# Kernel tuning notes

Hardware: AMD Instinct MI355X
Metric: run time of the kernel (lower is better)

Reference implementation:

```python
import jax, jax.numpy as jnp
import numpy as np

B, L, D_MODEL, D_STATE, D_CONV, EXPAND = 2, 1024, 1024, 16, 4, 2
D_INNER = D_MODEL * EXPAND


def setup_inputs() -> dict:
    key = jax.random.key(0)
    ks = jax.random.split(key, 8)
    s = lambda fan: 1.0 / np.sqrt(fan)
    x = jax.random.normal(ks[0], (B, L, D_MODEL), jnp.float32)
    in_proj_w = jax.random.normal(ks[1], (D_MODEL, 2 * D_INNER), jnp.float32) * s(D_MODEL)
    conv_w = jax.random.normal(ks[2], (D_INNER, 1, D_CONV), jnp.float32) * s(D_CONV)
    conv_b = jax.random.normal(ks[3], (D_INNER,), jnp.float32) * 0.01
    x_proj_w = jax.random.normal(ks[4], (D_INNER, 2 * D_STATE + D_INNER), jnp.float32) * s(D_INNER)
    dt_proj_w = jax.random.normal(ks[5], (D_INNER, D_INNER), jnp.float32) * s(D_INNER)
    dt_proj_b = jax.random.normal(ks[6], (D_INNER,), jnp.float32) * 0.01
    A_log = jnp.log(jnp.tile(jnp.arange(1, D_STATE + 1, dtype=jnp.float32)[None, :], (D_INNER, 1)))
    D = jnp.ones((D_INNER,), jnp.float32)
    out_proj_w = jax.random.normal(ks[7], (D_INNER, D_MODEL), jnp.float32) * s(D_INNER)
    return {"x": x, "in_proj_w": in_proj_w, "conv_w": conv_w, "conv_b": conv_b,
            "x_proj_w": x_proj_w, "dt_proj_w": dt_proj_w, "dt_proj_b": dt_proj_b,
            "A_log": A_log, "D": D, "out_proj_w": out_proj_w}


def _mamba_forward(x, in_proj_w, conv_w, conv_b, x_proj_w, dt_proj_w, dt_proj_b, A_log, D, out_proj_w):
    Bb, Ll, _ = x.shape
    d_inner, _, d_conv = conv_w.shape
    d_state = A_log.shape[1]
    # input projection and gate split
    xz = x @ in_proj_w                       # [B, L, 2*Di]
    x_inner, z = jnp.split(xz, 2, axis=-1)   # each [B, L, Di]
    # causal depthwise conv (left pad k-1, truncate to L == torch pad+slice)
    xc = jnp.transpose(x_inner, (0, 2, 1))   # [B, Di, L]
    xc = jax.lax.conv_general_dilated(
        xc, conv_w, window_strides=(1,), padding=[(d_conv - 1, 0)],
        dimension_numbers=("NCH", "OIH", "NCH"), feature_group_count=d_inner)
    xc = xc + conv_b[None, :, None]
    u = jax.nn.silu(jnp.transpose(xc, (0, 2, 1)))  # [B, L, Di]
    # SSM parameter projections
    ssm = u @ x_proj_w                        # [B, L, 2N+Di]
    B_ssm = ssm[..., :d_state]                # [B, L, N]
    C_ssm = ssm[..., d_state:2 * d_state]     # [B, L, N]
    dt = jax.nn.softplus(ssm[..., 2 * d_state:] @ dt_proj_w + dt_proj_b)  # [B, L, Di]
    A_real = -jnp.exp(A_log)                  # [Di, N]
    # selective scan over sequence (recurrence via lax.scan)
    def step(h, inp):
        dt_t, B_t, u_t = inp                  # [B,Di], [B,N], [B,Di]
        dA = jnp.exp(dt_t[..., None] * A_real)            # [B, Di, N]
        dBu = dt_t[..., None] * B_t[:, None, :] * u_t[..., None]
        h = dA * h + dBu
        return h, h
    h0 = jnp.zeros((Bb, d_inner, d_state), x.dtype)
    xs = (jnp.swapaxes(dt, 0, 1), jnp.swapaxes(B_ssm, 0, 1), jnp.swapaxes(u, 0, 1))
    _, states = jax.lax.scan(step, h0, xs)    # [L, B, Di, N]
    y = jnp.einsum("lbdn,lbn->lbd", states, jnp.swapaxes(C_ssm, 0, 1))
    y = jnp.swapaxes(y, 0, 1) + D * u         # skip connection
    y = y * jax.nn.silu(z)                    # gating
    return y @ out_proj_w                     # [B, L, d_model]


def reference(x, in_proj_w, conv_w, conv_b, x_proj_w, dt_proj_w, dt_proj_b, A_log, D, out_proj_w):
    return _mamba_forward(x, in_proj_w, conv_w, conv_b, x_proj_w, dt_proj_w, dt_proj_b, A_log, D, out_proj_w)
```

## Files before the change

kernel.cpp:

```cpp
#include <hip/hip_runtime.h>
#include <hip/hip_bf16.h>

#define BB 2
#define LL 1024
#define DMODEL 1024
#define DINNER 2048
#define DSTATE 16
#define DCONV 4
#define MM (BB * LL)
#define N_XZ 4096
#define N_SSM 2080
#define N_SSM_PAD 2176
#define CCH 32
#define LCH 32

typedef __hip_bfloat16 bf16;
typedef short bf16x8 __attribute__((ext_vector_type(8)));
typedef float f32x4 __attribute__((ext_vector_type(4)));

__device__ __forceinline__ void load16_lds(const bf16* g, bf16* l) {
    __builtin_amdgcn_global_load_lds(
        (const __attribute__((address_space(1))) void*)g,
        (__attribute__((address_space(3))) void*)l,
        16, 0, 0);
}

__global__ __launch_bounds__(256) void prep_kernel(
    const float* __restrict__ x, bf16* __restrict__ xbf,
    const float* __restrict__ w1, bf16* __restrict__ o1,
    const float* __restrict__ w2, bf16* __restrict__ o2,
    const float* __restrict__ w3, bf16* __restrict__ o3,
    const float* __restrict__ w4, bf16* __restrict__ o4)
{
    int bid = blockIdx.x;
    const float* src; bf16* dst; int K, N, tn, tk;
    if (bid < 4096)        { src = w1; dst = o1; K = 1024; N = 4096; tn = bid & 127; tk = bid >> 7; }
    else if (bid < 8256)   { bid -= 4096;  src = w2; dst = o2; K = 2048; N = 2080; tn = bid % 65; tk = bid / 65; }
    else if (bid < 12352)  { bid -= 8256;  src = w3; dst = o3; K = 2048; N = 2048; tn = bid & 63; tk = bid >> 6; }
    else if (bid < 14400)  { bid -= 12352; src = w4; dst = o4; K = 2048; N = 1024; tn = bid & 31; tk = bid >> 5; }
    else {
        bid -= 14400;
        int i = (bid * 256 + threadIdx.x) * 4;
        float4 v = *(const float4*)(x + i);
        xbf[i + 0] = __float2bfloat16(v.x);
        xbf[i + 1] = __float2bfloat16(v.y);
        xbf[i + 2] = __float2bfloat16(v.z);
        xbf[i + 3] = __float2bfloat16(v.w);
        return;
    }
    __shared__ float tile[32][33];
    const int nb = tn * 32, kb = tk * 32;
    const int tx = threadIdx.x & 31, ty = threadIdx.x >> 5;
    #pragma unroll
    for (int i = 0; i < 32; i += 8) {
        int k = kb + ty + i, n = nb + tx;
        tile[ty + i][tx] = (k < K && n < N) ? src[(size_t)k * N + n] : 0.f;
    }
    __syncthreads();
    #pragma unroll
    for (int i = 0; i < 32; i += 8) {
        int n = nb + ty + i, k = kb + tx;
        if (n < N && k < K) dst[(size_t)n * K + k] = __float2bfloat16(tile[tx][ty + i]);
    }
}

#define TM 128
#define TN 64
#define TK 64
template<int EPI, int KSPLIT = 1, int SWZ = -1>
__global__ __launch_bounds__(256) void mfma_gemm(
    const bf16* __restrict__ A, int lda,
    const bf16* __restrict__ Wt, int ldw,
    float* __restrict__ Cf, bf16* __restrict__ Cb, int ldc,
    const float* __restrict__ bias,
    int N, int K)
{
    __shared__ __align__(16) bf16 As[2][TM * TK];
    __shared__ __align__(16) bf16 Bs[2][TN * TK];
    const int tid = threadIdx.x;
    const int wave = tid >> 6, lane = tid & 63;
    const int wm = (wave >> 1) * 64, wn = (wave & 1) * 32;

    int bx, by;
    if (SWZ >= 0) {
        int id = blockIdx.x + (int)(gridDim.x * blockIdx.y);
        int xcd = id & 7, slot = id >> 3;
        bx = (xcd << SWZ) + (slot & ((1 << SWZ) - 1));
        by = slot >> SWZ;
    } else { bx = blockIdx.x; by = blockIdx.y; }
    const int m0 = by * TM, n0 = bx * TN;
    const int lm = lane & 15, kq = lane >> 4;

    const int srow = lane >> 3;
    const int schunk = (lane & 7) ^ srow;
    const bf16* gA = A + (size_t)(m0 + wave * 32 + srow) * lda + schunk * 8;
    const bf16* gB = Wt + (size_t)(n0 + wave * 16 + srow) * ldw + schunk * 8;

    const int Kc = K / KSPLIT;
    const int kbeg = (KSPLIT > 1) ? blockIdx.z * Kc : 0;
    const int NK = Kc / TK;

    f32x4 acc[4][2] = {};
    const int fsw = (lm & 7);

    auto stage = [&](int buf, int it) {
        const int k0 = kbeg + it * TK;
        bf16* lA = &As[buf][(wave * 32) * TK];
        bf16* lB = &Bs[buf][(wave * 16) * TK];
        #pragma unroll
        for (int g = 0; g < 4; ++g)
            load16_lds(gA + (size_t)(8 * g) * lda + k0, lA + (8 * g) * TK);
        #pragma unroll
        for (int g = 0; g < 2; ++g)
            load16_lds(gB + (size_t)(8 * g) * ldw + k0, lB + (8 * g) * TK);
    };
    auto compute = [&](int buf) {
        bf16x8 af[4][2], bfr[2][2];
        #pragma unroll
        for (int i = 0; i < 4; ++i)
            #pragma unroll
            for (int t = 0; t < 2; ++t)
                af[i][t] = *(const bf16x8*)(&As[buf][(wm + i * 16 + lm) * TK + ((t * 4 + kq) ^ fsw) * 8]);
        #pragma unroll
        for (int j = 0; j < 2; ++j)
            #pragma unroll
            for (int t = 0; t < 2; ++t)
                bfr[j][t] = *(const bf16x8*)(&Bs[buf][(wn + j * 16 + lm) * TK + ((t * 4 + kq) ^ fsw) * 8]);
        #pragma unroll
        for (int t = 0; t < 2; ++t)
            #pragma unroll
            for (int i = 0; i < 4; ++i)
                #pragma unroll
                for (int j = 0; j < 2; ++j)
                    acc[i][j] = __builtin_amdgcn_mfma_f32_16x16x32_bf16(af[i][t], bfr[j][t], acc[i][j], 0, 0, 0);
    };

    stage(0, 0);
    for (int it = 0; it < NK; it += 2) {
        stage(1, it + 1);
        __builtin_amdgcn_s_waitcnt(0x0F76);
        __builtin_amdgcn_s_barrier();
        compute(0);
        __builtin_amdgcn_s_barrier();
        if (it + 2 < NK) {
            stage(0, it + 2);
            __builtin_amdgcn_s_waitcnt(0x0F76);
        } else {
            __builtin_amdgcn_s_waitcnt(0x0F70);
        }
        __builtin_amdgcn_s_barrier();
        compute(1);
        __builtin_amdgcn_s_barrier();
    }

    #pragma unroll
    for (int i = 0; i < 4; ++i) {
        #pragma unroll
        for (int j = 0; j < 2; ++j) {
            int gcol = n0 + wn + j * 16 + lm;
            if ((EPI == 0 || EPI == 3) && gcol >= N) continue;
            #pragma unroll
            for (int r = 0; r < 4; ++r) {
                int grow = m0 + wm + i * 16 + kq * 4 + r;
                float v = acc[i][j][r];
                if (EPI == 1) {
                    v += bias[gcol];
                    v = (v > 20.f) ? v : log1pf(__expf(v));
                    Cf[(size_t)grow * ldc + gcol] = v;
                } else if (EPI == 2) {
                    if (KSPLIT > 1) atomicAdd(&Cf[(size_t)grow * ldc + gcol], v);
                    else            Cf[(size_t)grow * ldc + gcol] = v;
                } else if (EPI == 3) {
                    if (gcol < 32) Cf[(size_t)grow * 32 + gcol] = v;
                    else           Cb[(size_t)grow * ldc + gcol] = __float2bfloat16(v);
                } else {
                    Cb[(size_t)grow * ldc + gcol] = __float2bfloat16(v);
                }
            }
        }
    }
}

__global__ void conv_silu_kernel(const bf16* __restrict__ xz,
                                 const float* __restrict__ conv_w,
                                 const float* __restrict__ conv_b,
                                 bf16* __restrict__ u)
{
    int idx = blockIdx.x * blockDim.x + threadIdx.x;
    if (idx >= BB * LL * DINNER) return;
    int d = idx & (DINNER - 1);
    int l = (idx >> 11) & (LL - 1);
    int b = idx >> 21;
    float acc = conv_b[d];
    #pragma unroll
    for (int j = 0; j < DCONV; ++j) {
        int ll = l - (DCONV - 1) + j;
        if (ll >= 0) {
            float xv = (float)xz[((size_t)(b * LL + ll)) * N_XZ + d];
            acc = fmaf(conv_w[d * DCONV + j], xv, acc);
        }
    }
    u[idx] = __float2bfloat16(acc / (1.f + __expf(-acc)));
}

__global__ __launch_bounds__(256) void scan_phase_a(
    const float* __restrict__ dt, const bf16* __restrict__ u,
    const float* __restrict__ BC,
    const float* __restrict__ A_log,
    float* __restrict__ chunkP, float* __restrict__ chunkH)
{
    const int d = blockIdx.x * 256 + threadIdx.x;
    const int c = blockIdx.y, b = blockIdx.z;
    const int l0 = c * LCH;

    float A[DSTATE];
    {
        const f32x4* ap = (const f32x4*)(A_log + d * DSTATE);
        #pragma unroll
        for (int q = 0; q < 4; ++q) {
            f32x4 v = ap[q];
            #pragma unroll
            for (int r = 0; r < 4; ++r) A[q * 4 + r] = -__expf(v[r]);
        }
    }
    float h[DSTATE];
    #pragma unroll
    for (int n = 0; n < DSTATE; ++n) h[n] = 0.f;
    float sdt = 0.f;

    const float* dtp = dt + ((size_t)b * LL + l0) * DINNER + d;
    const bf16* up = u + ((size_t)b * LL + l0) * DINNER + d;
    const float* bcp = BC + ((size_t)b * LL + l0) * 32;

    #pragma unroll 2
    for (int i = 0; i < LCH; ++i) {
        float dtv = *dtp;
        float uv  = (float)*up;
        float du  = dtv * uv;
        f32x4 Bv[4];
        #pragma unroll
        for (int q = 0; q < 4; ++q) Bv[q] = *(const f32x4*)(bcp + q * 4);
        #pragma unroll
        for (int n = 0; n < DSTATE; ++n) {
            float a = __expf(dtv * A[n]);
            h[n] = fmaf(a, h[n], du * Bv[n >> 2][n & 3]);
        }
        sdt += dtv;
        dtp += DINNER; up += DINNER; bcp += 32;
    }

    size_t idx = (((size_t)b * CCH + c) * DINNER + d) * DSTATE;
    #pragma unroll
    for (int q = 0; q < 4; ++q) {
        f32x4 pv, hv;
        #pragma unroll
        for (int r = 0; r < 4; ++r) { pv[r] = __expf(A[q * 4 + r] * sdt); hv[r] = h[q * 4 + r]; }
        *(f32x4*)(chunkP + idx + q * 4) = pv;
        *(f32x4*)(chunkH + idx + q * 4) = hv;
    }
}

__global__ __launch_bounds__(256) void scan_phase_p(
    const float* __restrict__ chunkP, float* __restrict__ chunkH)
{
    int gid = blockIdx.x * 256 + threadIdx.x;
    int n = gid & 15;
    int d = (gid >> 4) & (DINNER - 1);
    int b = gid >> 15;
    const size_t stride = (size_t)DINNER * DSTATE;
    size_t idx = ((size_t)b * CCH * DINNER + d) * DSTATE + n;
    float H = 0.f;
    for (int c = 0; c < CCH; ++c) {
        float P  = chunkP[idx];
        float hl = chunkH[idx];
        chunkH[idx] = H;
        H = fmaf(P, H, hl);
        idx += stride;
    }
}

__global__ __launch_bounds__(256) void scan_phase_b(
    const float* __restrict__ dt, bf16* __restrict__ u,
    const float* __restrict__ BC, const bf16* __restrict__ xz,
    const float* __restrict__ A_log, const float* __restrict__ Dp,
    const float* __restrict__ chunkH)
{
    const int d = blockIdx.x * 256 + threadIdx.x;
    const int c = blockIdx.y, b = blockIdx.z;
    const int l0 = c * LCH;

    float A[DSTATE];
    {
        const f32x4* ap = (const f32x4*)(A_log + d * DSTATE);
        #pragma unroll
        for (int q = 0; q < 4; ++q) {
            f32x4 v = ap[q];
            #pragma unroll
            for (int r = 0; r < 4; ++r) A[q * 4 + r] = -__expf(v[r]);
        }
    }
    const float Dd = Dp[d];
    float h[DSTATE];
    {
        size_t idx = (((size_t)b * CCH + c) * DINNER + d) * DSTATE;
        #pragma unroll
        for (int q = 0; q < 4; ++q) {
            f32x4 v = *(const f32x4*)(chunkH + idx + q * 4);
            #pragma unroll
            for (int r = 0; r < 4; ++r) h[q * 4 + r] = v[r];
        }
    }

    const float* dtp = dt + ((size_t)b * LL + l0) * DINNER + d;
    bf16* up = u + ((size_t)b * LL + l0) * DINNER + d;
    const float* bcp = BC + ((size_t)b * LL + l0) * 32;
    const bf16* zp = xz + ((size_t)b * LL + l0) * N_XZ + DINNER + d;

    #pragma unroll 2
    for (int i = 0; i < LCH; ++i) {
        float dtv = *dtp;
        float uv  = (float)*up;
        float du  = dtv * uv;
        f32x4 Bv[4], Cv[4];
        #pragma unroll
        for (int q = 0; q < 4; ++q) {
            Bv[q] = *(const f32x4*)(bcp + q * 4);
            Cv[q] = *(const f32x4*)(bcp + 16 + q * 4);
        }
        float acc = 0.f;
        #pragma unroll
        for (int n = 0; n < DSTATE; ++n) {
            float a = __expf(dtv * A[n]);
            h[n] = fmaf(a, h[n], du * Bv[n >> 2][n & 3]);
            acc = fmaf(h[n], Cv[n >> 2][n & 3], acc);
        }
        float zv = (float)*zp;
        acc = fmaf(Dd, uv, acc);
        acc *= zv / (1.f + __expf(-zv));
        *up = __float2bfloat16(acc);
        dtp += DINNER; up += DINNER; bcp += 32; zp += N_XZ;
    }
}

extern "C" void kernel_launch(void* const* d_in, const int* in_sizes, int n_in,
                              void* d_out, int out_size, void* d_ws, size_t ws_size,
                              hipStream_t stream) {
    const float* x         = (const float*)d_in[0];
    const float* in_proj_w = (const float*)d_in[1];
    const float* conv_w    = (const float*)d_in[2];
    const float* conv_b    = (const float*)d_in[3];
    const float* x_proj_w  = (const float*)d_in[4];
    const float* dt_proj_w = (const float*)d_in[5];
    const float* dt_proj_b = (const float*)d_in[6];
    const float* A_log     = (const float*)d_in[7];
    const float* Dp        = (const float*)d_in[8];
    const float* out_proj_w= (const float*)d_in[9];
    float* out = (float*)d_out;

    char* p = (char*)d_ws;
    float* dt   = (float*)p;                          p += (size_t)MM * DINNER * 4;
    bf16*  xbf  = (bf16*)dt;
    bf16*  xz   = (bf16*)p;                           p += (size_t)MM * N_XZ * 2;
    bf16*  u    = (bf16*)p;                           p += (size_t)MM * DINNER * 2;
    bf16*  ssm  = (bf16*)p;                           p += (size_t)MM * N_SSM * 2;
    bf16*  Wt1  = (bf16*)p;                           p += (size_t)N_XZ * DMODEL * 2;
    bf16*  Wt2  = (bf16*)p;                           p += (size_t)N_SSM_PAD * DINNER * 2;
    bf16*  Wt3  = (bf16*)p;                           p += (size_t)DINNER * DINNER * 2;
    bf16*  Wt4  = (bf16*)p;                           p += (size_t)DMODEL * DINNER * 2;
    float* BC   = (float*)p;                          p += (size_t)MM * 32 * 4;
    float* chunkP = (float*)Wt1;
    float* chunkH = (float*)Wt2;

    prep_kernel<<<16448, 256, 0, stream>>>(x, xbf, in_proj_w, Wt1, x_proj_w, Wt2,
                                           dt_proj_w, Wt3, out_proj_w, Wt4);
    mfma_gemm<0, 1, 3><<<dim3(N_XZ / TN, MM / TM), 256, 0, stream>>>(
        xbf, DMODEL, Wt1, DMODEL, nullptr, xz, N_XZ, nullptr, N_XZ, DMODEL);
    {
        int n = BB * LL * DINNER;
        conv_silu_kernel<<<(n + 255) / 256, 256, 0, stream>>>(xz, conv_w, conv_b, u);
    }
    mfma_gemm<3><<<dim3(N_SSM_PAD / TN, MM / TM), 256, 0, stream>>>(
        u, DINNER, Wt2, DINNER, BC, ssm, N_SSM, nullptr, N_SSM, DINNER);
    mfma_gemm<1, 1, 2><<<dim3(DINNER / TN, MM / TM), 256, 0, stream>>>(
        ssm + 2 * DSTATE, N_SSM, Wt3, DINNER, dt, nullptr, DINNER, dt_proj_b, DINNER, DINNER);
    scan_phase_a<<<dim3(DINNER / 256, CCH, BB), 256, 0, stream>>>(dt, u, BC, A_log, chunkP, chunkH);
    scan_phase_p<<<dim3(BB * DINNER * DSTATE / 256), 256, 0, stream>>>(chunkP, chunkH);
    scan_phase_b<<<dim3(DINNER / 256, CCH, BB), 256, 0, stream>>>(dt, u, BC, xz, A_log, Dp, chunkH);
    hipMemsetAsync(out, 0, (size_t)out_size * sizeof(float), stream);
    mfma_gemm<2, 2, 1><<<dim3(DMODEL / TN, MM / TM, 2), 256, 0, stream>>>(
        u, DINNER, Wt4, DINNER, out, nullptr, DMODEL, nullptr, DMODEL, DINNER);
}
```

Baseline: 332.9 us.

## Use 2-wave GEMM blocks with 64x64 warp tiles and vectorize conv

The GEMM now runs two waves per block instead of four. Each wave computes a 64x64 sub-tile, so each wave issues more MFMAs per LDS fragment load and gets more register-level reuse. Each wave now stages twice as many global-to-LDS loads, and the waitcnt thresholds change to match. The depthwise conv+SiLU kernel is also vectorized to process 8 channels per thread with 16-byte loads and stores. The trade-off is higher register pressure and fewer waves per block for latency hiding.

```diff
diff --git a/kernel.cpp b/kernel.cpp
--- a/kernel.cpp
+++ b/kernel.cpp
@@ -68,7 +68,7 @@
 #define TN 64
 #define TK 64
 template<int EPI, int KSPLIT = 1, int SWZ = -1>
-__global__ __launch_bounds__(256) void mfma_gemm(
+__global__ __launch_bounds__(128) void mfma_gemm(
     const bf16* __restrict__ A, int lda,
     const bf16* __restrict__ Wt, int ldw,
     float* __restrict__ Cf, bf16* __restrict__ Cb, int ldc,
@@ -79,7 +79,7 @@
     __shared__ __align__(16) bf16 Bs[2][TN * TK];
     const int tid = threadIdx.x;
     const int wave = tid >> 6, lane = tid & 63;
-    const int wm = (wave >> 1) * 64, wn = (wave & 1) * 32;
+    const int wm = wave * 64;
 
     int bx, by;
     if (SWZ >= 0) {
@@ -93,58 +93,58 @@
 
     const int srow = lane >> 3;
     const int schunk = (lane & 7) ^ srow;
-    const bf16* gA = A + (size_t)(m0 + wave * 32 + srow) * lda + schunk * 8;
-    const bf16* gB = Wt + (size_t)(n0 + wave * 16 + srow) * ldw + schunk * 8;
+    const bf16* gA = A + (size_t)(m0 + wave * 64 + srow) * lda + schunk * 8;
+    const bf16* gB = Wt + (size_t)(n0 + wave * 32 + srow) * ldw + schunk * 8;
 
     const int Kc = K / KSPLIT;
     const int kbeg = (KSPLIT > 1) ? blockIdx.z * Kc : 0;
     const int NK = Kc / TK;
 
-    f32x4 acc[4][2] = {};
+    f32x4 acc[4][4] = {};
     const int fsw = (lm & 7);
 
     auto stage = [&](int buf, int it) {
         const int k0 = kbeg + it * TK;
-        bf16* lA = &As[buf][(wave * 32) * TK];
-        bf16* lB = &Bs[buf][(wave * 16) * TK];
+        bf16* lA = &As[buf][(wave * 64) * TK];
+        bf16* lB = &Bs[buf][(wave * 32) * TK];
+        #pragma unroll
+        for (int g = 0; g < 8; ++g)
+            load16_lds(gA + (size_t)(8 * g) * lda + k0, lA + (8 * g) * TK);
         #pragma unroll
         for (int g = 0; g < 4; ++g)
-            load16_lds(gA + (size_t)(8 * g) * lda + k0, lA + (8 * g) * TK);
-        #pragma unroll
-        for (int g = 0; g < 2; ++g)
             load16_lds(gB + (size_t)(8 * g) * ldw + k0, lB + (8 * g) * TK);
     };
     auto compute = [&](int buf) {
-        bf16x8 af[4][2], bfr[2][2];
+        bf16x8 af[4][2], bfr[4][2];
         #pragma unroll
         for (int i = 0; i < 4; ++i)
             #pragma unroll
             for (int t = 0; t < 2; ++t)
                 af[i][t] = *(const bf16x8*)(&As[buf][(wm + i * 16 + lm) * TK + ((t * 4 + kq) ^ fsw) * 8]);
         #pragma unroll
-        for (int j = 0; j < 2; ++j)
+        for (int j = 0; j < 4; ++j)
             #pragma unroll
             for (int t = 0; t < 2; ++t)
-                bfr[j][t] = *(const bf16x8*)(&Bs[buf][(wn + j * 16 + lm) * TK + ((t * 4 + kq) ^ fsw) * 8]);
+                bfr[j][t] = *(const bf16x8*)(&Bs[buf][(j * 16 + lm) * TK + ((t * 4 + kq) ^ fsw) * 8]);
         #pragma unroll
         for (int t = 0; t < 2; ++t)
             #pragma unroll
             for (int i = 0; i < 4; ++i)
                 #pragma unroll
-                for (int j = 0; j < 2; ++j)
+                for (int j = 0; j < 4; ++j)
                     acc[i][j] = __builtin_amdgcn_mfma_f32_16x16x32_bf16(af[i][t], bfr[j][t], acc[i][j], 0, 0, 0);
     };
 
     stage(0, 0);
     for (int it = 0; it < NK; it += 2) {
         stage(1, it + 1);
-        __builtin_amdgcn_s_waitcnt(0x0F76);
+        __builtin_amdgcn_s_waitcnt(0x0F7C);
         __builtin_amdgcn_s_barrier();
         compute(0);
         __builtin_amdgcn_s_barrier();
         if (it + 2 < NK) {
             stage(0, it + 2);
-            __builtin_amdgcn_s_waitcnt(0x0F76);
+            __builtin_amdgcn_s_waitcnt(0x0F7C);
         } else {
             __builtin_amdgcn_s_waitcnt(0x0F70);
         }
@@ -156,8 +156,8 @@
     #pragma unroll
     for (int i = 0; i < 4; ++i) {
         #pragma unroll
-        for (int j = 0; j < 2; ++j) {
-            int gcol = n0 + wn + j * 16 + lm;
+        for (int j = 0; j < 4; ++j) {
+            int gcol = n0 + j * 16 + lm;
             if ((EPI == 0 || EPI == 3) && gcol >= N) continue;
             #pragma unroll
             for (int r = 0; r < 4; ++r) {
@@ -187,20 +187,38 @@
                                  bf16* __restrict__ u)
 {
     int idx = blockIdx.x * blockDim.x + threadIdx.x;
-    if (idx >= BB * LL * DINNER) return;
-    int d = idx & (DINNER - 1);
-    int l = (idx >> 11) & (LL - 1);
-    int b = idx >> 21;
-    float acc = conv_b[d];
+    int d8 = idx & (DINNER / 8 - 1);
+    int l  = (idx >> 8) & (LL - 1);
+    int b  = idx >> 18;
+    int d0 = d8 * 8;
+
+    float acc[8];
+    {
+        float4 b0 = *(const float4*)(conv_b + d0);
+        float4 b1 = *(const float4*)(conv_b + d0 + 4);
+        acc[0] = b0.x; acc[1] = b0.y; acc[2] = b0.z; acc[3] = b0.w;
+        acc[4] = b1.x; acc[5] = b1.y; acc[6] = b1.z; acc[7] = b1.w;
+    }
     #pragma unroll
     for (int j = 0; j < DCONV; ++j) {
         int ll = l - (DCONV - 1) + j;
         if (ll >= 0) {
-            float xv = (float)xz[((size_t)(b * LL + ll)) * N_XZ + d];
-            acc = fmaf(conv_w[d * DCONV + j], xv, acc);
-        }
-    }
-    u[idx] = __float2bfloat16(acc / (1.f + __expf(-acc)));
+            bf16x8 v = *(const bf16x8*)(xz + ((size_t)(b * LL + ll)) * N_XZ + d0);
+            #pragma unroll
+            for (int r = 0; r < 8; ++r) {
+                float xv = __uint_as_float(((unsigned)(unsigned short)v[r]) << 16);
+                acc[r] = fmaf(conv_w[(d0 + r) * DCONV + j], xv, acc[r]);
+            }
+        }
+    }
+    bf16x8 out;
+    #pragma unroll
+    for (int r = 0; r < 8; ++r) {
+        float y = acc[r] / (1.f + __expf(-acc[r]));
+        bf16 h = __float2bfloat16(y);
+        out[r] = *reinterpret_cast<short*>(&h);
+    }
+    *(bf16x8*)(u + ((size_t)(b * LL + l)) * DINNER + d0) = out;
 }
 
 __global__ __launch_bounds__(256) void scan_phase_a(
@@ -373,20 +391,20 @@
 
     prep_kernel<<<16448, 256, 0, stream>>>(x, xbf, in_proj_w, Wt1, x_proj_w, Wt2,
                                            dt_proj_w, Wt3, out_proj_w, Wt4);
-    mfma_gemm<0, 1, 3><<<dim3(N_XZ / TN, MM / TM), 256, 0, stream>>>(
+    mfma_gemm<0, 1, 3><<<dim3(N_XZ / TN, MM / TM), 128, 0, stream>>>(
         xbf, DMODEL, Wt1, DMODEL, nullptr, xz, N_XZ, nullptr, N_XZ, DMODEL);
     {
-        int n = BB * LL * DINNER;
+        int n = BB * LL * DINNER / 8;
         conv_silu_kernel<<<(n + 255) / 256, 256, 0, stream>>>(xz, conv_w, conv_b, u);
     }
-    mfma_gemm<3><<<dim3(N_SSM_PAD / TN, MM / TM), 256, 0, stream>>>(
+    mfma_gemm<3><<<dim3(N_SSM_PAD / TN, MM / TM), 128, 0, stream>>>(
         u, DINNER, Wt2, DINNER, BC, ssm, N_SSM, nullptr, N_SSM, DINNER);
-    mfma_gemm<1, 1, 2><<<dim3(DINNER / TN, MM / TM), 256, 0, stream>>>(
+    mfma_gemm<1, 1, 2><<<dim3(DINNER / TN, MM / TM), 128, 0, stream>>>(
         ssm + 2 * DSTATE, N_SSM, Wt3, DINNER, dt, nullptr, DINNER, dt_proj_b, DINNER, DINNER);
     scan_phase_a<<<dim3(DINNER / 256, CCH, BB), 256, 0, stream>>>(dt, u, BC, A_log, chunkP, chunkH);
     scan_phase_p<<<dim3(BB * DINNER * DSTATE / 256), 256, 0, stream>>>(chunkP, chunkH);
     scan_phase_b<<<dim3(DINNER / 256, CCH, BB), 256, 0, stream>>>(dt, u, BC, xz, A_log, Dp, chunkH);
     hipMemsetAsync(out, 0, (size_t)out_size * sizeof(float), stream);
-    mfma_gemm<2, 2, 1><<<dim3(DMODEL / TN, MM / TM, 2), 256, 0, stream>>>(
+    mfma_gemm<2, 2, 1><<<dim3(DMODEL / TN, MM / TM, 2), 128, 0, stream>>>(
         u, DINNER, Wt4, DINNER, out, nullptr, DMODEL, nullptr, DMODEL, DINNER);
 }
```

Measured after the change: 384.9 us. 15.6% more time.

## Triple-buffer GEMM LDS pipeline and vectorize conv+SiLU kernel

Applied to the files above, without the earlier changes.

The shared MFMA GEMM goes from a two-stage to a three-stage LDS ring. Loads run up to two K-tiles ahead and the waitcnt thresholds are adjusted to match, so global-load latency is hidden better. This raises LDS use per block (from 48KB to 72KB), which may reduce occupancy. Separately, the depthwise conv+SiLU kernel now handles 8 channels per thread with 16-byte vector loads and stores, cutting the thread count and the number of memory instructions.

```diff
diff --git a/kernel.cpp b/kernel.cpp
--- a/kernel.cpp
+++ b/kernel.cpp
@@ -75,8 +75,8 @@
     const float* __restrict__ bias,
     int N, int K)
 {
-    __shared__ __align__(16) bf16 As[2][TM * TK];
-    __shared__ __align__(16) bf16 Bs[2][TN * TK];
+    __shared__ __align__(16) bf16 As[3][TM * TK];
+    __shared__ __align__(16) bf16 Bs[3][TN * TK];
     const int tid = threadIdx.x;
     const int wave = tid >> 6, lane = tid & 63;
     const int wm = (wave >> 1) * 64, wn = (wave & 1) * 32;
@@ -135,22 +135,16 @@
                     acc[i][j] = __builtin_amdgcn_mfma_f32_16x16x32_bf16(af[i][t], bfr[j][t], acc[i][j], 0, 0, 0);
     };
 
-    stage(0, 0);
-    for (int it = 0; it < NK; it += 2) {
-        stage(1, it + 1);
-        __builtin_amdgcn_s_waitcnt(0x0F76);
+    stage(0, 0); stage(1, 1); stage(2, 2);
+    for (int it = 0; it < NK; ++it) {
+        if (it + 2 < NK)      __builtin_amdgcn_s_waitcnt(0x0F7C);
+        else if (it + 1 < NK) __builtin_amdgcn_s_waitcnt(0x0F76);
+        else                  __builtin_amdgcn_s_waitcnt(0x0F70);
         __builtin_amdgcn_s_barrier();
-        compute(0);
+        const int buf = it % 3;
+        compute(buf);
         __builtin_amdgcn_s_barrier();
-        if (it + 2 < NK) {
-            stage(0, it + 2);
-            __builtin_amdgcn_s_waitcnt(0x0F76);
-        } else {
-            __builtin_amdgcn_s_waitcnt(0x0F70);
-        }
-        __builtin_amdgcn_s_barrier();
-        compute(1);
-        __builtin_amdgcn_s_barrier();
+        if (it + 3 < NK) stage(buf, it + 3);
     }
 
     #pragma unroll
@@ -187,20 +181,38 @@
                                  bf16* __restrict__ u)
 {
     int idx = blockIdx.x * blockDim.x + threadIdx.x;
-    if (idx >= BB * LL * DINNER) return;
-    int d = idx & (DINNER - 1);
-    int l = (idx >> 11) & (LL - 1);
-    int b = idx >> 21;
-    float acc = conv_b[d];
+    int d8 = idx & (DINNER / 8 - 1);
+    int l  = (idx >> 8) & (LL - 1);
+    int b  = idx >> 18;
+    int d0 = d8 * 8;
+
+    float acc[8];
+    {
+        float4 b0 = *(const float4*)(conv_b + d0);
+        float4 b1 = *(const float4*)(conv_b + d0 + 4);
+        acc[0] = b0.x; acc[1] = b0.y; acc[2] = b0.z; acc[3] = b0.w;
+        acc[4] = b1.x; acc[5] = b1.y; acc[6] = b1.z; acc[7] = b1.w;
+    }
     #pragma unroll
     for (int j = 0; j < DCONV; ++j) {
         int ll = l - (DCONV - 1) + j;
         if (ll >= 0) {
-            float xv = (float)xz[((size_t)(b * LL + ll)) * N_XZ + d];
-            acc = fmaf(conv_w[d * DCONV + j], xv, acc);
-        }
-    }
-    u[idx] = __float2bfloat16(acc / (1.f + __expf(-acc)));
+            bf16x8 v = *(const bf16x8*)(xz + ((size_t)(b * LL + ll)) * N_XZ + d0);
+            #pragma unroll
+            for (int r = 0; r < 8; ++r) {
+                float xv = __uint_as_float(((unsigned)(unsigned short)v[r]) << 16);
+                acc[r] = fmaf(conv_w[(d0 + r) * DCONV + j], xv, acc[r]);
+            }
+        }
+    }
+    bf16x8 out;
+    #pragma unroll
+    for (int r = 0; r < 8; ++r) {
+        float y = acc[r] / (1.f + __expf(-acc[r]));
+        bf16 h = __float2bfloat16(y);
+        out[r] = *reinterpret_cast<short*>(&h);
+    }
+    *(bf16x8*)(u + ((size_t)(b * LL + l)) * DINNER + d0) = out;
 }
 
 __global__ __launch_bounds__(256) void scan_phase_a(
@@ -376,7 +388,7 @@
     mfma_gemm<0, 1, 3><<<dim3(N_XZ / TN, MM / TM), 256, 0, stream>>>(
         xbf, DMODEL, Wt1, DMODEL, nullptr, xz, N_XZ, nullptr, N_XZ, DMODEL);
     {
-        int n = BB * LL * DINNER;
+        int n = BB * LL * DINNER / 8;
         conv_silu_kernel<<<(n + 255) / 256, 256, 0, stream>>>(xz, conv_w, conv_b, u);
     }
     mfma_gemm<3><<<dim3(N_SSM_PAD / TN, MM / TM), 256, 0, stream>>>(
```

Result: slower. 363.4 us (+9.2%).
